# Kernel tuning notes

Measured on AMD Instinct MI355X. Metric: run time of the kernel, lower is better.

The kernel has to match this reference:

```python
import jax, jax.numpy as jnp
import numpy as np

B, M, L, LQ, E, V = 32, 100, 30, 30, 256, 32000


def position_encoding(seq_len, emb):
    # faithful to MemN2N position encoding: 1 + 4*(k - (E+1)/2)*(j - (J+1)/2)/(E*J)
    j = jnp.arange(1, seq_len + 1, dtype=jnp.float32)[:, None]   # (J,1)
    k = jnp.arange(1, emb + 1, dtype=jnp.float32)[None, :]       # (1,E)
    half_e = (emb + 1) / 2.0
    half_j = (seq_len + 1) / 2.0
    return 1.0 + 4.0 * (k - half_e) * (j - half_j) / (emb * seq_len)  # (J,E)


def masked_softmax(x, m):
    xm = jnp.where(m > 0, x, -1e30)
    e = jnp.exp(xm - jnp.max(xm, axis=-1, keepdims=True)) * m
    return e / (jnp.sum(e, axis=-1, keepdims=True) + 1e-13)


def masked_log_softmax(x, m):
    return jax.nn.log_softmax(x + jnp.log(m + 1e-13), axis=-1)


def _forward(trainS, trainQ, trainVM, trainPM, trainSM, trainQM,
             A1, A2, A3, A4, W, b, gamma, beta):
    # query encoding: embed + position encode + query mask + sum over words
    Q = trainQ[:, 0, :]                                   # (B,LQ)
    pe_q = position_encoding(LQ, E)                       # (LQ,E)
    u = jnp.sum(A1[Q] * pe_q * trainQM[:, :, None], axis=1)  # (B,E)

    # story memory embeddings: gather + PE + sum over words.
    # NOTE: original code multiplies by trainSM but discards the result (bug),
    # so SM is intentionally NOT applied here.
    pe_s = position_encoding(L, E)                        # (L,E)
    embA1 = jnp.sum(A1[trainS] * pe_s, axis=2)            # (B,M,E)
    embA2 = jnp.sum(A2[trainS] * pe_s, axis=2)
    embA3 = jnp.sum(A3[trainS] * pe_s, axis=2)
    embA4 = jnp.sum(A4[trainS] * pe_s, axis=2)

    def hop(memA, memC, u):
        # scores = sum_E(memA * u) * PM (PM applied pre-sum is equivalent)
        scores = jnp.einsum('bme,be->bm', memA, u) * trainPM
        p = masked_softmax(scores, trainPM)               # (B,M)
        o = jnp.einsum('bm,bme->be', p, memC)             # (B,E)
        return o + u

    u = hop(embA1, embA2, u)   # hop 1
    u = hop(embA2, embA3, u)   # hop 2
    u = hop(embA3, embA4, u)   # hop 3

    # final linear + BatchNorm1d (training-mode batch stats, eps=1e-5)
    wx = u @ W.T + b                                      # (B,V)
    mean = jnp.mean(wx, axis=0)
    var = jnp.mean((wx - mean) ** 2, axis=0)
    y = gamma * (wx - mean) / jnp.sqrt(var + 1e-5) + beta
    return masked_log_softmax(y, trainVM)


def setup_inputs() -> dict:
    key = jax.random.key(0)
    ks = jax.random.split(key, 8)
    inp = {
        'trainS': jax.random.randint(ks[0], (B, M, L), 0, V, dtype=jnp.int32),
        'trainQ': jax.random.randint(ks[1], (B, 1, LQ), 0, V, dtype=jnp.int32),
        'trainVM': jnp.ones((B, V), jnp.float32),
        'trainPM': jnp.ones((B, M), jnp.float32),
        'trainSM': jnp.ones((B, M, L), jnp.float32),
        'trainQM': jnp.ones((B, LQ), jnp.float32),
        'A1': 0.1 * jax.random.normal(ks[2], (V, E), jnp.float32),
        'A2': 0.1 * jax.random.normal(ks[3], (V, E), jnp.float32),
        'A3': 0.1 * jax.random.normal(ks[4], (V, E), jnp.float32),
        'A4': 0.1 * jax.random.normal(ks[5], (V, E), jnp.float32),
        'W': jax.random.normal(ks[6], (V, E), jnp.float32) / np.sqrt(E),
        'b': jnp.zeros((V,), jnp.float32),
        'gamma': jnp.ones((V,), jnp.float32),
        'beta': jnp.zeros((V,), jnp.float32),
        'inspect': 0,
    }
    return inp


def reference(trainS, trainQ, trainVM, trainPM, trainSM, trainQM,
              A1, A2, A3, A4, W, b, gamma, beta, inspect):
    return _forward(trainS, trainQ, trainVM, trainPM, trainSM, trainQM,
                    A1, A2, A3, A4, W, b, gamma, beta)
```

## Files before the change

kernel.cpp:

```cpp
#include <hip/hip_runtime.h>
#include <math.h>

static constexpr int B_ = 32, M_ = 100, L_ = 30, LQ_ = 30, E_ = 256, V_ = 32000;

typedef __attribute__((ext_vector_type(8))) short bf16x8;
typedef __attribute__((ext_vector_type(4))) float f32x4;

__device__ __forceinline__ unsigned f2bf(float f) {
    unsigned u = __float_as_uint(f);
    return (u + 0x7FFFu + ((u >> 16) & 1u)) >> 16;
}

__global__ __launch_bounds__(256) void k_embed(const int* __restrict__ trainS,
                                               const float* __restrict__ A1,
                                               const float* __restrict__ A2,
                                               const float* __restrict__ A3,
                                               const float* __restrict__ A4,
                                               float* __restrict__ embA) {
    const int bm = blockIdx.x;
    const int tbl = threadIdx.x >> 6;
    const int e0 = (threadIdx.x & 63) * 4;
    const float* __restrict__ A = (tbl == 0) ? A1 : (tbl == 1) ? A2 : (tbl == 2) ? A3 : A4;
    const float half_e = (E_ + 1) * 0.5f;
    const float half_j = (L_ + 1) * 0.5f;
    const float inv = 1.0f / (float)(E_ * L_);
    const float k0 = (float)(e0 + 1) - half_e;
    const float k1 = k0 + 1.f, k2 = k0 + 2.f, k3 = k0 + 3.f;

    int idx[L_];
#pragma unroll
    for (int l = 0; l < L_; ++l) idx[l] = trainS[bm * L_ + l];

    float4 acc = make_float4(0.f, 0.f, 0.f, 0.f);
#pragma unroll
    for (int c = 0; c < 2; ++c) {
        float4 r[15];
#pragma unroll
        for (int j = 0; j < 15; ++j)
            r[j] = *reinterpret_cast<const float4*>(A + (size_t)idx[c * 15 + j] * E_ + e0);
        __builtin_amdgcn_sched_barrier(0);
#pragma unroll
        for (int j = 0; j < 15; ++j) {
            const int l = c * 15 + j;
            const float coef = 4.0f * ((float)(l + 1) - half_j) * inv;
            acc.x += r[j].x * (1.0f + coef * k0);
            acc.y += r[j].y * (1.0f + coef * k1);
            acc.z += r[j].z * (1.0f + coef * k2);
            acc.w += r[j].w * (1.0f + coef * k3);
        }
    }
    *reinterpret_cast<float4*>(embA + (size_t)tbl * (B_ * M_ * E_) + (size_t)bm * E_ + e0) = acc;
}

__global__ __launch_bounds__(1024) void k_hops(const int* __restrict__ trainQ,
                                               const float* __restrict__ trainQM,
                                               const float* __restrict__ A1,
                                               const float* __restrict__ embA,
                                               const float* __restrict__ trainPM,
                                               float* __restrict__ u_N,
                                               float* __restrict__ partial) {
    const int b = blockIdx.x;
    const int tid = threadIdx.x;
    const int lane = tid & 63;
    const int wave = tid >> 6;
    const int g = tid >> 8;
    const int e = tid & 255;
    if (tid < 8) partial[b * 8 + tid] = 0.f;
    __shared__ float u_sh[E_];
    __shared__ float sc[M_];
    __shared__ float p_sh[M_];
    __shared__ float osum[4][E_];

    {
        const float half_e = (E_ + 1) * 0.5f;
        const float half_j = (LQ_ + 1) * 0.5f;
        const float inv = 1.0f / (float)(E_ * LQ_);
        const float ke = (float)(e + 1) - half_e;
        const int l0 = g * 8;
        const int ln = (LQ_ - l0 < 8) ? (LQ_ - l0) : 8;
        int qi[8];
        float qm[8];
#pragma unroll
        for (int j = 0; j < 8; ++j) {
            if (j < ln) {
                qi[j] = trainQ[b * LQ_ + l0 + j];
                qm[j] = trainQM[b * LQ_ + l0 + j];
            } else { qi[j] = 0; qm[j] = 0.f; }
        }
        float r[8];
#pragma unroll
        for (int j = 0; j < 8; ++j)
            r[j] = (j < ln) ? A1[(size_t)qi[j] * E_ + e] : 0.f;
        float part = 0.f;
#pragma unroll
        for (int j = 0; j < 8; ++j) {
            const float pe = 1.0f + 4.0f * ke * ((float)(l0 + j + 1) - half_j) * inv;
            part += r[j] * pe * qm[j];
        }
        osum[g][e] = part;
    }
    __syncthreads();
    if (tid < E_) u_sh[tid] = osum[0][tid] + osum[1][tid] + osum[2][tid] + osum[3][tid];
    __syncthreads();

    for (int hop = 0; hop < 3; ++hop) {
        const float* memA = embA + (size_t)hop * (B_ * M_ * E_) + (size_t)b * M_ * E_;
        const float* memC = memA + (size_t)(B_ * M_ * E_);

        float rv[7][4];
#pragma unroll
        for (int t = 0; t < 7; ++t) {
            const int m = wave + t * 16;
            if (m < M_) {
                const float* row = memA + (size_t)m * E_;
#pragma unroll
                for (int j = 0; j < 4; ++j) rv[t][j] = row[lane + 64 * j];
            }
        }
        __builtin_amdgcn_sched_barrier(0);
#pragma unroll
        for (int t = 0; t < 7; ++t) {
            const int m = wave + t * 16;
            if (m < M_) {
                float part = rv[t][0] * u_sh[lane] + rv[t][1] * u_sh[lane + 64]
                           + rv[t][2] * u_sh[lane + 128] + rv[t][3] * u_sh[lane + 192];
#pragma unroll
                for (int off = 32; off > 0; off >>= 1)
                    part += __shfl_xor(part, off, 64);
                if (lane == 0) sc[m] = part * trainPM[b * M_ + m];
            }
        }

        float cv[25];
        {
            const float* crow = memC + e;
            const int m0 = g * 25;
#pragma unroll
            for (int mm = 0; mm < 25; ++mm)
                cv[mm] = crow[(size_t)(m0 + mm) * E_];
        }
        __builtin_amdgcn_sched_barrier(0);
        __syncthreads();

        if (wave == 0) {
            const float pm0 = (lane < M_) ? trainPM[b * M_ + lane] : 0.f;
            const float pm1 = (lane + 64 < M_) ? trainPM[b * M_ + lane + 64] : 0.f;
            const float x0 = (lane < M_ && pm0 > 0.f) ? sc[lane] : -1e30f;
            const float x1 = (lane + 64 < M_ && pm1 > 0.f) ? sc[lane + 64] : -1e30f;
            float mx = fmaxf(x0, x1);
#pragma unroll
            for (int off = 32; off > 0; off >>= 1)
                mx = fmaxf(mx, __shfl_xor(mx, off, 64));
            const float e0v = (lane < M_) ? expf(x0 - mx) * pm0 : 0.f;
            const float e1v = (lane + 64 < M_) ? expf(x1 - mx) * pm1 : 0.f;
            float ssum = e0v + e1v;
#pragma unroll
            for (int off = 32; off > 0; off >>= 1)
                ssum += __shfl_xor(ssum, off, 64);
            const float invs = 1.0f / (ssum + 1e-13f);
            if (lane < M_) p_sh[lane] = e0v * invs;
            if (lane + 64 < M_) p_sh[lane + 64] = e1v * invs;
        }
        __syncthreads();

        {
            float acc = 0.f;
            const int m0 = g * 25;
#pragma unroll
            for (int mm = 0; mm < 25; ++mm)
                acc += p_sh[m0 + mm] * cv[mm];
            osum[g][e] = acc;
        }
        __syncthreads();
        if (tid < E_) u_sh[tid] += osum[0][tid] + osum[1][tid] + osum[2][tid] + osum[3][tid];
        __syncthreads();
    }
    if (tid < E_) u_N[b * E_ + tid] = u_sh[tid];
}

__global__ __launch_bounds__(256) void k_output(const float* __restrict__ u_N,
                                                const float* __restrict__ Wm,
                                                const float* __restrict__ gamma,
                                                const float* __restrict__ beta,
                                                const float* __restrict__ VM,
                                                float* __restrict__ z,
                                                float* __restrict__ partial) {
    __shared__ char uAraw[32 * 512];
    __shared__ float pex[B_];
    const int tid = threadIdx.x;
    {
        const int m = tid >> 3;
        const int kc = (tid & 7) * 32;
        const float4* src = reinterpret_cast<const float4*>(u_N + m * E_ + kc);
#pragma unroll
        for (int j = 0; j < 4; ++j) {
            const float4 f0 = src[2 * j];
            const float4 f1 = src[2 * j + 1];
            uint4 q;
            q.x = f2bf(f0.x) | (f2bf(f0.y) << 16);
            q.y = f2bf(f0.z) | (f2bf(f0.w) << 16);
            q.z = f2bf(f1.x) | (f2bf(f1.y) << 16);
            q.w = f2bf(f1.z) | (f2bf(f1.w) << 16);
            const int k16 = kc / 8 + j;
            const int off = m * 512 + ((k16 * 16) ^ ((m & 7) << 4));
            *reinterpret_cast<uint4*>(uAraw + off) = q;
        }
    }
    if (tid < B_) pex[tid] = 0.f;
    __syncthreads();

    const int lane = tid & 63;
    const int wv = tid >> 6;
    const int col = lane & 15;
    const int grp = lane >> 4;
    const int n0 = (blockIdx.x * 4 + wv) * 16;
    const int v = n0 + col;

    float4 wreg[16];
    {
        const float* wrow = Wm + (size_t)v * E_ + grp * 8;
#pragma unroll
        for (int s = 0; s < 8; ++s) {
            wreg[2 * s] = *reinterpret_cast<const float4*>(wrow + s * 32);
            wreg[2 * s + 1] = *reinterpret_cast<const float4*>(wrow + s * 32 + 4);
        }
    }
    __builtin_amdgcn_sched_barrier(0);

    bf16x8 af[2][8];
#pragma unroll
    for (int mt = 0; mt < 2; ++mt) {
        const int m = mt * 16 + col;
#pragma unroll
        for (int s = 0; s < 8; ++s) {
            const int k16 = s * 4 + grp;
            const int off = m * 512 + ((k16 * 16) ^ ((m & 7) << 4));
            af[mt][s] = *reinterpret_cast<bf16x8*>(uAraw + off);
        }
    }

    f32x4 acc0 = {0.f, 0.f, 0.f, 0.f};
    f32x4 acc1 = {0.f, 0.f, 0.f, 0.f};
#pragma unroll
    for (int s = 0; s < 8; ++s) {
        const float4 w0 = wreg[2 * s], w1 = wreg[2 * s + 1];
        bf16x8 bf;
        bf[0] = (short)f2bf(w0.x); bf[1] = (short)f2bf(w0.y);
        bf[2] = (short)f2bf(w0.z); bf[3] = (short)f2bf(w0.w);
        bf[4] = (short)f2bf(w1.x); bf[5] = (short)f2bf(w1.y);
        bf[6] = (short)f2bf(w1.z); bf[7] = (short)f2bf(w1.w);
        acc0 = __builtin_amdgcn_mfma_f32_16x16x32_bf16(af[0][s], bf, acc0, 0, 0, 0);
        acc1 = __builtin_amdgcn_mfma_f32_16x16x32_bf16(af[1][s], bf, acc1, 0, 0, 0);
    }

    float s1 = 0.f, s2 = 0.f;
#pragma unroll
    for (int r = 0; r < 4; ++r) {
        s1 += acc0[r] + acc1[r];
        s2 += acc0[r] * acc0[r] + acc1[r] * acc1[r];
    }
    s1 += __shfl_xor(s1, 16, 64);
    s2 += __shfl_xor(s2, 16, 64);
    s1 += __shfl_xor(s1, 32, 64);
    s2 += __shfl_xor(s2, 32, 64);
    const float mean = s1 * (1.0f / B_);
    const float var = s2 * (1.0f / B_) - mean * mean;
    const float rstd = rsqrtf(var + 1e-5f);
    const float gg = gamma[v], be = beta[v];

#pragma unroll
    for (int mt = 0; mt < 2; ++mt) {
#pragma unroll
        for (int r = 0; r < 4; ++r) {
            const int b = mt * 16 + grp * 4 + r;
            const float wx = (mt == 0) ? acc0[r] : acc1[r];
            const float y = gg * (wx - mean) * rstd + be;
            const size_t row = (size_t)b * V_ + v;
            const float vm = VM[row] + 1e-13f;
            z[row] = y + logf(vm);
            atomicAdd(&pex[b], vm * expf(y));
        }
    }
    __syncthreads();
    if (tid < B_) atomicAdd(&partial[tid * 8 + (blockIdx.x & 7)], pex[tid]);
}

__global__ __launch_bounds__(256) void k_final(const float* __restrict__ z,
                                               const float* __restrict__ partial,
                                               float* __restrict__ out) {
    const int idx = blockIdx.x * 256 + threadIdx.x;
    const int b = idx / (V_ / 4);
    const int v4 = idx % (V_ / 4);
    float s = 0.f;
#pragma unroll
    for (int k = 0; k < 8; ++k) s += partial[b * 8 + k];
    const float lse = logf(s);
    const float4 x = reinterpret_cast<const float4*>(z + (size_t)b * V_)[v4];
    float4 o;
    o.x = x.x - lse; o.y = x.y - lse; o.z = x.z - lse; o.w = x.w - lse;
    reinterpret_cast<float4*>(out + (size_t)b * V_)[v4] = o;
}

extern "C" void kernel_launch(void* const* d_in, const int* in_sizes, int n_in,
                              void* d_out, int out_size, void* d_ws, size_t ws_size,
                              hipStream_t stream) {
    const int* trainS = (const int*)d_in[0];
    const int* trainQ = (const int*)d_in[1];
    const float* trainVM = (const float*)d_in[2];
    const float* trainPM = (const float*)d_in[3];
    const float* trainQM = (const float*)d_in[5];
    const float* A1 = (const float*)d_in[6];
    const float* A2 = (const float*)d_in[7];
    const float* A3 = (const float*)d_in[8];
    const float* A4 = (const float*)d_in[9];
    const float* Wm = (const float*)d_in[10];
    const float* gamma = (const float*)d_in[12];
    const float* beta = (const float*)d_in[13];
    float* out = (float*)d_out;

    float* ws = (float*)d_ws;
    float* u_N = ws;
    float* embA = ws + 8192;
    float* z = embA + 4 * (B_ * M_ * E_);
    float* partial = z + (size_t)B_ * V_;

    k_embed<<<B_ * M_, 256, 0, stream>>>(trainS, A1, A2, A3, A4, embA);
    k_hops<<<B_, 1024, 0, stream>>>(trainQ, trainQM, A1, embA, trainPM, u_N, partial);
    k_output<<<V_ / 64, 256, 0, stream>>>(u_N, Wm, gamma, beta, trainVM, z, partial);
    k_final<<<(B_ * V_ / 4) / 256, 256, 0, stream>>>(z, partial, out);
}
```

Baseline: 105.8 us.

## Fuse log-softmax normalization into output kernel via cooperative grid sync

Merges the final log-softmax subtraction kernel into the output GEMM kernel. Per-element z and exp values stay in registers, a cooperative grid barrier waits for all partial sums, and each block then writes the normalized output directly. This drops the intermediate z round-trip through global memory and one kernel launch. The per-element shared atomics are also replaced by wave shuffle reductions before a single atomic per row group. The cost is a cooperative launch of 500 blocks with a grid-wide barrier, which requires every block to be co-resident and adds sync latency.

```diff
diff --git a/kernel.cpp b/kernel.cpp
--- a/kernel.cpp
+++ b/kernel.cpp
@@ -1,5 +1,8 @@
 #include <hip/hip_runtime.h>
+#include <hip/hip_cooperative_groups.h>
 #include <math.h>
+
+namespace cg = cooperative_groups;
 
 static constexpr int B_ = 32, M_ = 100, L_ = 30, LQ_ = 30, E_ = 256, V_ = 32000;
 
@@ -183,10 +186,11 @@
                                                 const float* __restrict__ gamma,
                                                 const float* __restrict__ beta,
                                                 const float* __restrict__ VM,
-                                                float* __restrict__ z,
+                                                float* __restrict__ out,
                                                 float* __restrict__ partial) {
     __shared__ char uAraw[32 * 512];
     __shared__ float pex[B_];
+    __shared__ float lse_sh[B_];
     const int tid = threadIdx.x;
     {
         const int m = tid >> 3;
@@ -268,6 +272,7 @@
     const float rstd = rsqrtf(var + 1e-5f);
     const float gg = gamma[v], be = beta[v];
 
+    float zr[2][4], ex[2][4];
 #pragma unroll
     for (int mt = 0; mt < 2; ++mt) {
 #pragma unroll
@@ -275,30 +280,47 @@
             const int b = mt * 16 + grp * 4 + r;
             const float wx = (mt == 0) ? acc0[r] : acc1[r];
             const float y = gg * (wx - mean) * rstd + be;
-            const size_t row = (size_t)b * V_ + v;
-            const float vm = VM[row] + 1e-13f;
-            z[row] = y + logf(vm);
-            atomicAdd(&pex[b], vm * expf(y));
-        }
+            const float vm = VM[(size_t)b * V_ + v] + 1e-13f;
+            zr[mt][r] = y + logf(vm);
+            ex[mt][r] = vm * expf(y);
+        }
+    }
+#pragma unroll
+    for (int off = 1; off < 16; off <<= 1) {
+#pragma unroll
+        for (int mt = 0; mt < 2; ++mt)
+#pragma unroll
+            for (int r = 0; r < 4; ++r)
+                ex[mt][r] += __shfl_xor(ex[mt][r], off, 64);
+    }
+    if (col == 0) {
+#pragma unroll
+        for (int mt = 0; mt < 2; ++mt)
+#pragma unroll
+            for (int r = 0; r < 4; ++r)
+                atomicAdd(&pex[mt * 16 + grp * 4 + r], ex[mt][r]);
     }
     __syncthreads();
     if (tid < B_) atomicAdd(&partial[tid * 8 + (blockIdx.x & 7)], pex[tid]);
-}
-
-__global__ __launch_bounds__(256) void k_final(const float* __restrict__ z,
-                                               const float* __restrict__ partial,
-                                               float* __restrict__ out) {
-    const int idx = blockIdx.x * 256 + threadIdx.x;
-    const int b = idx / (V_ / 4);
-    const int v4 = idx % (V_ / 4);
-    float s = 0.f;
-#pragma unroll
-    for (int k = 0; k < 8; ++k) s += partial[b * 8 + k];
-    const float lse = logf(s);
-    const float4 x = reinterpret_cast<const float4*>(z + (size_t)b * V_)[v4];
-    float4 o;
-    o.x = x.x - lse; o.y = x.y - lse; o.z = x.z - lse; o.w = x.w - lse;
-    reinterpret_cast<float4*>(out + (size_t)b * V_)[v4] = o;
+
+    cg::this_grid().sync();
+
+    if (tid < B_) {
+        float s = 0.f;
+#pragma unroll
+        for (int k = 0; k < 8; ++k) s += partial[tid * 8 + k];
+        lse_sh[tid] = logf(s);
+    }
+    __syncthreads();
+
+#pragma unroll
+    for (int mt = 0; mt < 2; ++mt) {
+#pragma unroll
+        for (int r = 0; r < 4; ++r) {
+            const int b = mt * 16 + grp * 4 + r;
+            out[(size_t)b * V_ + v] = zr[mt][r] - lse_sh[b];
+        }
+    }
 }
 
 extern "C" void kernel_launch(void* const* d_in, const int* in_sizes, int n_in,
@@ -321,11 +343,12 @@
     float* ws = (float*)d_ws;
     float* u_N = ws;
     float* embA = ws + 8192;
-    float* z = embA + 4 * (B_ * M_ * E_);
-    float* partial = z + (size_t)B_ * V_;
+    float* partial = embA + 4 * (B_ * M_ * E_);
 
     k_embed<<<B_ * M_, 256, 0, stream>>>(trainS, A1, A2, A3, A4, embA);
     k_hops<<<B_, 1024, 0, stream>>>(trainQ, trainQM, A1, embA, trainPM, u_N, partial);
-    k_output<<<V_ / 64, 256, 0, stream>>>(u_N, Wm, gamma, beta, trainVM, z, partial);
-    k_final<<<(B_ * V_ / 4) / 256, 256, 0, stream>>>(z, partial, out);
-}
+
+    void* kargs[] = {(void*)&u_N, (void*)&Wm, (void*)&gamma, (void*)&beta,
+                     (void*)&trainVM, (void*)&out, (void*)&partial};
+    hipLaunchCooperativeKernel((void*)k_output, dim3(V_ / 64), dim3(256), kargs, 0, stream);
+}
```

Measured after the change: 135.9 us. 28.5% more time.
